# Kernel optimization log

Measured on AMD Instinct MI355X. Metric: run time of the kernel, lower is better.

## Reference

```python
import jax, jax.numpy as jnp
import numpy as np

B, S, D, H, F, E = 2, 1024, 1024, 16, 2048, 8
HD = D // H


def _ln(x, g, b, eps=1e-5):
    m = x.mean(-1, keepdims=True)
    v = ((x - m) ** 2).mean(-1, keepdims=True)
    return (x - m) / jnp.sqrt(v + eps) * g + b


def setup_inputs() -> dict:
    key = jax.random.key(0)
    ks = jax.random.split(key, 12)
    rn = lambda k, shp, s=0.02: jax.random.normal(k, shp, jnp.float32) * s
    return {
        'src': jax.random.normal(ks[0], (B, S, D), jnp.float32),
        'q_w': rn(ks[1], (D, D)),
        'k_w': rn(ks[2], (D, D)),
        'v_w': rn(ks[3], (D, D)),
        'out_w': rn(ks[4], (D, D)),
        'gate_w': rn(ks[5], (D, D)),
        'gate_b': rn(ks[6], (D,)),
        'scale_w': rn(ks[7], (H, HD)),
        'n1_g': jnp.ones((D,), jnp.float32),
        'n1_b': jnp.zeros((D,), jnp.float32),
        'n2_g': jnp.ones((D,), jnp.float32),
        'n2_b': jnp.zeros((D,), jnp.float32),
        'moe_gate_w': rn(ks[8], (D, E)),
        'moe_gate_b': jnp.zeros((E,), jnp.float32),
        'w1': rn(ks[9], (E, D, F)),
        'b1': jnp.zeros((E, F), jnp.float32),
        'ln_g': jnp.ones((E, F), jnp.float32),
        'ln_b': jnp.zeros((E, F), jnp.float32),
        'w2': rn(ks[10], (E, F, D)),
        'b2': jnp.zeros((E, D), jnp.float32),
        'res_scale': jnp.ones((E,), jnp.float32),
    }


def reference(src, q_w, k_w, v_w, out_w, gate_w, gate_b, scale_w,
              n1_g, n1_b, n2_g, n2_b, moe_gate_w, moe_gate_b,
              w1, b1, ln_g, ln_b, w2, b2, res_scale):
    b, s, d = src.shape
    h = scale_w.shape[0]
    hd = d // h
    # --- MemoAttention (gated, dynamically scaled), eval mode ---
    q = (src @ q_w).reshape(b, s, h, hd).transpose(0, 2, 1, 3)  # [b,h,s,hd]
    k = (src @ k_w).reshape(b, s, h, hd).transpose(0, 2, 1, 3)
    v = (src @ v_w).reshape(b, s, h, hd).transpose(0, 2, 1, 3)
    scores = jnp.einsum('bhqd,bhkd->bhqk', q, k) / np.float32(np.sqrt(hd))
    scale = jax.nn.sigmoid(jnp.einsum('bhsd,hd->bhs', q, scale_w)) * 2.0
    scores = scores * scale[..., None]
    aw = jax.nn.softmax(scores, axis=-1)
    out = jnp.einsum('bhqk,bhkd->bhqd', aw, v).transpose(0, 2, 1, 3).reshape(b, s, d)
    gate = jax.nn.sigmoid(out @ gate_w + gate_b)
    attn = (out * gate) @ out_w
    # --- residual + norm1 ---
    x = _ln(src + attn, n1_g, n1_b)
    # --- MoE FFN (top-2 routing; torch loop overwrites -> last (max-index) expert
    xr = x.reshape(-1, d)                      # [N, d]
    n = xr.shape[0]
    logits = xr @ moe_gate_w + moe_gate_b       # [N, E]
    top_v, top_i = jax.lax.top_k(logits, 2)
    wts = jax.nn.softmax(top_v, axis=-1)        # [N, 2]
    chosen = jnp.max(top_i, axis=-1)            # last-written expert per token

    def expert(W1, B1, G, Bt, W2, B2, rsc):
        hh = xr @ W1 + B1                       # [N, F]
        hh = jax.nn.gelu(_ln(hh, G, Bt), approximate=False)
        return (hh @ W2 + B2) * rsc + xr        # [N, d]

    outs = jax.vmap(expert)(w1, b1, ln_g, ln_b, w2, b2, res_scale)  # [E,N,d]
    sel = jnp.take_along_axis(outs.transpose(1, 0, 2), chosen[:, None, None], axis=1)[:, 0]
    moe = sel * jnp.sum(wts, axis=-1, keepdims=True)
    # --- residual + norm2 ---
    return _ln(x + moe.reshape(b, s, d), n2_g, n2_b)
```

## Files before the change

kernel.cpp:

```cpp
#include <hip/hip_runtime.h>


typedef _Float16 f16;
typedef _Float16 f16x8 __attribute__((ext_vector_type(8)));
typedef _Float16 f16x4 __attribute__((ext_vector_type(4)));
typedef float f32x4 __attribute__((ext_vector_type(4)));

constexpr int CS  = 1024;
constexpr int CD  = 1024;
constexpr int CH  = 16;
constexpr int CHD = 64;
constexpr int CF  = 2048;
constexpr int CE  = 8;
constexpr int CN  = 2048;
constexpr int CBH = 32;
constexpr int KS  = 512;
constexpr int MAXT = 48;

constexpr float LO_SCALE = 2048.f;
constexpr float LO_INV   = 1.f / 2048.f;

#define MFMA16(a, b, c) __builtin_amdgcn_mfma_f32_16x16x32_f16((a), (b), (c), 0, 0, 0)

#define TO_GBL(p) ((const __attribute__((address_space(1))) void*)(p))
#define TO_LDS(p) ((__attribute__((address_space(3))) void*)(p))
#define GLD16(g, l) __builtin_amdgcn_global_load_lds(TO_GBL(g), TO_LDS(l), 16, 0, 0)

__device__ __forceinline__ void fsplit(float v, f16 &hi, f16 &lo) {
  hi = (f16)v;
  lo = (f16)((v - (float)hi) * LO_SCALE);
}


__global__ void k_split_cvt(const float* __restrict__ in, f16* __restrict__ oh,
                            f16* __restrict__ ol, int n) {
  int i = (blockIdx.x * blockDim.x + threadIdx.x) * 4;
  if (i >= n) return;
  float4 v = *(const float4*)(in + i);
  float a[4] = {v.x, v.y, v.z, v.w};
#pragma unroll
  for (int j = 0; j < 4; ++j) {
    f16 hi = (f16)a[j];
    oh[i + j] = hi;
    ol[i + j] = (f16)((a[j] - (float)hi) * LO_SCALE);
  }
}

__global__ void k_transpose_split(const float* __restrict__ in, f16* __restrict__ oh,
                                  f16* __restrict__ ol, int R, int C) {
  __shared__ float t[32][33];
  const int z = blockIdx.z;
  const float* src = in + (size_t)z * R * C;
  f16* dh = oh + (size_t)z * R * C;
  f16* dl = ol ? ol + (size_t)z * R * C : nullptr;
  const int c0 = blockIdx.x * 32, r0 = blockIdx.y * 32;
  const int tx = threadIdx.x, ty = threadIdx.y;
#pragma unroll
  for (int i = 0; i < 32; i += 8)
    t[ty + i][tx] = src[(size_t)(r0 + ty + i) * C + c0 + tx];
  __syncthreads();
#pragma unroll
  for (int i = 0; i < 32; i += 8) {
    float v = t[tx][ty + i];
    f16 hi = (f16)v;
    size_t idx = (size_t)(c0 + ty + i) * R + r0 + tx;
    dh[idx] = hi;
    if (dl) dl[idx] = (f16)((v - (float)hi) * LO_SCALE);
  }
}


template <bool SPLIT>
__device__ __forceinline__ void gemm_tile_db(
    const f16* aH, const f16* aL, const f16* bH, const f16* bL,
    size_t bRowStride , int K, f16* lds,
    f32x4 (&accm)[2][4], f32x4 (&accc)[2][4]) {
  constexpr int BUF = SPLIT ? 12288 : 6144;
  constexpr int BOFF = SPLIT ? 4096 : 2048;
  const int t = threadIdx.x;
  const int lane = t & 63, wave = t >> 6;
  const int wm = wave >> 1, wn = wave & 1;
  const int m16 = lane & 15, quad = lane >> 4;
  int aoff[2], boff[4];
#pragma unroll
  for (int sm = 0; sm < 2; ++sm) {
    const int r = wm * 32 + sm * 16 + m16;
    aoff[sm] = r * 32 + ((quad ^ ((r >> 1) & 3)) * 8);
  }
#pragma unroll
  for (int sn = 0; sn < 4; ++sn) {
    const int r = wn * 64 + sn * 16 + m16;
    boff[sn] = BOFF + r * 32 + ((quad ^ ((r >> 1) & 3)) * 8);
  }
  auto stage = [&](f16* buf) {
    GLD16(aH, buf + t * 8);
    GLD16(bH, buf + BOFF + t * 8);
    GLD16(bH + bRowStride, buf + BOFF + 2048 + t * 8);
    if constexpr (SPLIT) {
      GLD16(aL, buf + 2048 + t * 8);
      GLD16(bL, buf + 8192 + t * 8);
      GLD16(bL + bRowStride, buf + 10240 + t * 8);
      aL += 32; bL += 32;
    }
    aH += 32; bH += 32;
  };
  stage(lds);
  int cur = 0;
  for (int k = 0; k < K; k += 32) {
    __syncthreads();
    f16* buf = lds + cur * BUF;
    if (k + 32 < K) stage(lds + (cur ^ 1) * BUF);
    f16x8 af[2], alf[2], bf[4], blf[4];
#pragma unroll
    for (int sm = 0; sm < 2; ++sm) {
      af[sm] = *(const f16x8*)(buf + aoff[sm]);
      if constexpr (SPLIT) alf[sm] = *(const f16x8*)(buf + 2048 + aoff[sm]);
    }
#pragma unroll
    for (int sn = 0; sn < 4; ++sn) {
      bf[sn] = *(const f16x8*)(buf + boff[sn]);
      if constexpr (SPLIT) blf[sn] = *(const f16x8*)(buf + 4096 + boff[sn]);
    }
#pragma unroll
    for (int sm = 0; sm < 2; ++sm)
#pragma unroll
      for (int sn = 0; sn < 4; ++sn) {
        accm[sm][sn] = MFMA16(af[sm], bf[sn], accm[sm][sn]);
        if constexpr (SPLIT) {
          accc[sm][sn] = MFMA16(af[sm], blf[sn], accc[sm][sn]);
          accc[sm][sn] = MFMA16(alf[sm], bf[sn], accc[sm][sn]);
        }
      }
    cur ^= 1;
  }
}


__global__ __launch_bounds__(256) void g_qkv(
    const f16* __restrict__ srcH, const f16* __restrict__ srcL,
    const f16* __restrict__ qwH, const f16* __restrict__ qwL,
    const f16* __restrict__ kwH, const f16* __restrict__ kwL,
    const f16* __restrict__ vwH, const f16* __restrict__ vwL,
    f16* __restrict__ qHo, f16* __restrict__ qLo,
    f16* __restrict__ kHo, f16* __restrict__ kLo,
    f16* __restrict__ vTH, f16* __restrict__ vTL) {
  __shared__ f16 lds[24576];
  const int z = blockIdx.z;
  const int m0 = blockIdx.x * 64, n0 = blockIdx.y * 128;
  const int t = threadIdx.x;
  const int rowS = t >> 2;
  const int ksw = ((t & 3) ^ ((rowS >> 1) & 3)) * 8;
  const f16* BH = (z == 0) ? qwH : (z == 1) ? kwH : vwH;
  const f16* BL = (z == 0) ? qwL : (z == 1) ? kwL : vwL;
  const f32x4 VZ = {0.f, 0.f, 0.f, 0.f};
  f32x4 accm[2][4], accc[2][4];
#pragma unroll
  for (int i = 0; i < 2; ++i)
#pragma unroll
    for (int j = 0; j < 4; ++j) { accm[i][j] = VZ; accc[i][j] = VZ; }
  gemm_tile_db<true>(srcH + (size_t)(m0 + rowS) * CD + ksw,
                     srcL + (size_t)(m0 + rowS) * CD + ksw,
                     BH + (size_t)(n0 + rowS) * CD + ksw,
                     BL + (size_t)(n0 + rowS) * CD + ksw,
                     (size_t)64 * CD, CD, lds, accm, accc);
  const int lane = t & 63, wave = t >> 6;
  const int wm = wave >> 1, wn = wave & 1;
  const int m16 = lane & 15, quad = lane >> 4;
#pragma unroll
  for (int sm = 0; sm < 2; ++sm)
#pragma unroll
    for (int sn = 0; sn < 4; ++sn)
#pragma unroll
      for (int r = 0; r < 4; ++r) {
        const int row = m0 + wm * 32 + sm * 16 + quad * 4 + r;
        const int col = n0 + wn * 64 + sn * 16 + m16;
        const float v = accm[sm][sn][r] + accc[sm][sn][r] * LO_INV;
        f16 hi, lo; fsplit(v, hi, lo);
        const int bb = row >> 10, ss = row & 1023;
        const int hh = col >> 6, hd = col & 63;
        if (z == 2) {
          const size_t idx = ((size_t)((bb * CH + hh) * CHD + hd)) * CS + ss;
          vTH[idx] = hi; vTL[idx] = lo;
        } else {
          const size_t idx = ((size_t)((bb * CH + hh) * CS + ss)) * CHD + hd;
          if (z == 0) { qHo[idx] = hi; qLo[idx] = lo; }
          else        { kHo[idx] = hi; kLo[idx] = lo; }
        }
      }
}


__device__ __forceinline__ int pswz(int q, int k) {
  return q * 64 + ((((k >> 2) ^ q) & 15) << 2) + (k & 3);
}

__global__ __launch_bounds__(256) void k_fattn(
    const f16* __restrict__ qH_, const f16* __restrict__ qL_,
    const f16* __restrict__ kH_, const f16* __restrict__ kL_,
    const f16* __restrict__ vTH_, const f16* __restrict__ vTL_,
    const float* __restrict__ scale_w,
    f16* __restrict__ aoH, f16* __restrict__ aoL) {
  __shared__ f16 kvb[32768];
  __shared__ float psc[4 * 1024];
  const int bh = blockIdx.y;
  const int b = bh >> 4, h = bh & 15;
  const int t = threadIdx.x;
  const int lane = t & 63, wave = t >> 6;
  const int m16 = lane & 15, quad = lane >> 4;
  const int q0 = blockIdx.x * 64 + wave * 16;
  float* P = psc + wave * 1024;
  const f32x4 VZ = {0.f, 0.f, 0.f, 0.f};
  const size_t kb = (size_t)bh * CS * CHD;

  const int rowS = t >> 3, chS = t & 7;
  auto stage = [&](f16* dst, int kc) {
#pragma unroll
    for (int i = 0; i < 2; ++i) {
      const int row = rowS + 32 * i;
      const int sc = (chS ^ (row & 7)) * 8;
      GLD16(kH_ + kb + (size_t)(kc + row) * CHD + sc, dst + i * 2048 + t * 8);
      GLD16(kL_ + kb + (size_t)(kc + row) * CHD + sc, dst + 4096 + i * 2048 + t * 8);
      GLD16(vTH_ + kb + (size_t)row * CS + kc + sc, dst + 8192 + i * 2048 + t * 8);
      GLD16(vTL_ + kb + (size_t)row * CS + kc + sc, dst + 12288 + i * 2048 + t * 8);
    }
  };
  auto ldf = [&](const f16* piece, int r, int q) -> f16x8 {
    return *(const f16x8*)(piece + r * 64 + ((q ^ (r & 7)) * 8));
  };

  const f16* qrh = qH_ + ((size_t)bh * CS + q0 + m16) * CHD + quad * 8;
  const f16* qrl = qL_ + ((size_t)bh * CS + q0 + m16) * CHD + quad * 8;
  f16x8 a0h = *(const f16x8*)(qrh);
  f16x8 a1h = *(const f16x8*)(qrh + 32);
  f16x8 a0l = *(const f16x8*)(qrl);
  f16x8 a1l = *(const f16x8*)(qrl + 32);

  stage(kvb, 0);

  float dot = 0.f;
  {
    const float* sw = scale_w + h * CHD + quad * 8;
    float4 s0 = *(const float4*)(sw);
    float4 s1 = *(const float4*)(sw + 4);
    float4 s2 = *(const float4*)(sw + 32);
    float4 s3 = *(const float4*)(sw + 36);
    float sv[16] = {s0.x, s0.y, s0.z, s0.w, s1.x, s1.y, s1.z, s1.w,
                    s2.x, s2.y, s2.z, s2.w, s3.x, s3.y, s3.z, s3.w};
#pragma unroll
    for (int j = 0; j < 8; ++j) {
      dot += ((float)a0h[j] + (float)a0l[j] * LO_INV) * sv[j];
      dot += ((float)a1h[j] + (float)a1l[j] * LO_INV) * sv[8 + j];
    }
    dot += __shfl_xor(dot, 16);
    dot += __shfl_xor(dot, 32);
  }
  const float qsv = 2.f / (1.f + __expf(-dot));
  float qsr[4];
#pragma unroll
  for (int r = 0; r < 4; ++r) qsr[r] = __shfl(qsv, quad * 4 + r) * 0.125f;

  f32x4 accm[4], accc[4];
#pragma unroll
  for (int tt = 0; tt < 4; ++tt) { accm[tt] = VZ; accc[tt] = VZ; }
  float mrun[4], lrun[4];
#pragma unroll
  for (int r = 0; r < 4; ++r) { mrun[r] = -1e30f; lrun[r] = 0.f; }

  int cur = 0;
  for (int kc = 0; kc < CS; kc += 64) {
    __syncthreads();
    const f16* kv = kvb + cur * 16384;
    if (kc + 64 < CS) stage(kvb + (cur ^ 1) * 16384, kc + 64);

    f32x4 st[4];
#pragma unroll
    for (int tt = 0; tt < 4; ++tt) {
      const int r = tt * 16 + m16;
      f16x8 b0h = ldf(kv,        r, quad);
      f16x8 b1h = ldf(kv,        r, quad + 4);
      f16x8 b0l = ldf(kv + 4096, r, quad);
      f16x8 b1l = ldf(kv + 4096, r, quad + 4);
      f32x4 am = VZ, ac = VZ;
      am = MFMA16(a0h, b0h, am); am = MFMA16(a1h, b1h, am);
      ac = MFMA16(a0h, b0l, ac); ac = MFMA16(a0l, b0h, ac);
      ac = MFMA16(a1h, b1l, ac); ac = MFMA16(a1l, b1h, ac);
#pragma unroll
      for (int r4 = 0; r4 < 4; ++r4)
        st[tt][r4] = (am[r4] + ac[r4] * LO_INV) * qsr[r4];
    }
    float alpha[4];
#pragma unroll
    for (int r = 0; r < 4; ++r) {
      float mx = fmaxf(fmaxf(st[0][r], st[1][r]), fmaxf(st[2][r], st[3][r]));
#pragma unroll
      for (int msk = 8; msk >= 1; msk >>= 1) mx = fmaxf(mx, __shfl_xor(mx, msk));
      const float mnew = fmaxf(mrun[r], mx);
      alpha[r] = __expf(mrun[r] - mnew);
      mrun[r] = mnew;
    }
    float rs[4] = {0.f, 0.f, 0.f, 0.f};
#pragma unroll
    for (int tt = 0; tt < 4; ++tt)
#pragma unroll
      for (int r = 0; r < 4; ++r) {
        const float e = __expf(st[tt][r] - mrun[r]);
        rs[r] += e;
        P[pswz(quad * 4 + r, tt * 16 + m16)] = e;
      }
#pragma unroll
    for (int r = 0; r < 4; ++r) {
#pragma unroll
      for (int msk = 8; msk >= 1; msk >>= 1) rs[r] += __shfl_xor(rs[r], msk);
      lrun[r] = lrun[r] * alpha[r] + rs[r];
#pragma unroll
      for (int tt = 0; tt < 4; ++tt) { accm[tt][r] *= alpha[r]; accc[tt][r] *= alpha[r]; }
    }
    f16x8 pah[2], pal[2];
#pragma unroll
    for (int c = 0; c < 2; ++c) {
      const int k0 = c * 32 + quad * 8;
      float4 p0 = *(const float4*)(P + pswz(m16, k0));
      float4 p1 = *(const float4*)(P + pswz(m16, k0 + 4));
      float pv[8] = {p0.x, p0.y, p0.z, p0.w, p1.x, p1.y, p1.z, p1.w};
#pragma unroll
      for (int j = 0; j < 8; ++j) {
        f16 hi = (f16)pv[j];
        pah[c][j] = hi;
        pal[c][j] = (f16)((pv[j] - (float)hi) * LO_SCALE);
      }
    }
#pragma unroll
    for (int tt = 0; tt < 4; ++tt) {
      const int r = tt * 16 + m16;
#pragma unroll
      for (int c = 0; c < 2; ++c) {
        f16x8 vbh = ldf(kv + 8192,  r, quad + 4 * c);
        f16x8 vbl = ldf(kv + 12288, r, quad + 4 * c);
        accm[tt] = MFMA16(pah[c], vbh, accm[tt]);
        accc[tt] = MFMA16(pah[c], vbl, accc[tt]);
        accc[tt] = MFMA16(pal[c], vbh, accc[tt]);
      }
    }
    cur ^= 1;
  }
#pragma unroll
  for (int tt = 0; tt < 4; ++tt)
#pragma unroll
    for (int r = 0; r < 4; ++r) {
      const int row = q0 + quad * 4 + r;
      const float v = (accm[tt][r] + accc[tt][r] * LO_INV) / lrun[r];
      f16 hi, lo; fsplit(v, hi, lo);
      const size_t idx = ((size_t)(b * CS + row)) * CD + h * CHD + tt * 16 + m16;
      aoH[idx] = hi; aoL[idx] = lo;
    }
}


__global__ __launch_bounds__(256) void g_gate(
    const f16* __restrict__ aoH, const f16* __restrict__ aoL,
    const f16* __restrict__ gwH, const f16* __restrict__ gwL,
    float* __restrict__ gpre ) {
  __shared__ f16 lds[24576];
  const int m0 = blockIdx.x * 64, n0 = blockIdx.y * 128, s = blockIdx.z;
  const int t = threadIdx.x;
  const int rowS = t >> 2;
  const int ksw = ((t & 3) ^ ((rowS >> 1) & 3)) * 8;
  const int k0 = s * KS;
  const f32x4 VZ = {0.f, 0.f, 0.f, 0.f};
  f32x4 accm[2][4], accc[2][4];
#pragma unroll
  for (int i = 0; i < 2; ++i)
#pragma unroll
    for (int j = 0; j < 4; ++j) { accm[i][j] = VZ; accc[i][j] = VZ; }
  gemm_tile_db<true>(aoH + (size_t)(m0 + rowS) * CD + k0 + ksw,
                     aoL + (size_t)(m0 + rowS) * CD + k0 + ksw,
                     gwH + (size_t)(n0 + rowS) * CD + k0 + ksw,
                     gwL + (size_t)(n0 + rowS) * CD + k0 + ksw,
                     (size_t)64 * CD, KS, lds, accm, accc);
  float* gp = gpre + (size_t)s * CN * CD;
  const int lane = t & 63, wave = t >> 6;
  const int wm = wave >> 1, wn = wave & 1;
  const int m16 = lane & 15, quad = lane >> 4;
#pragma unroll
  for (int sm = 0; sm < 2; ++sm)
#pragma unroll
    for (int sn = 0; sn < 4; ++sn)
#pragma unroll
      for (int r = 0; r < 4; ++r) {
        const int row = m0 + wm * 32 + sm * 16 + quad * 4 + r;
        const int col = n0 + wn * 64 + sn * 16 + m16;
        gp[(size_t)row * CD + col] = accm[sm][sn][r] + accc[sm][sn][r] * LO_INV;
      }
}

__global__ __launch_bounds__(256) void k_gatemul(
    const float* __restrict__ gpre, const f16* __restrict__ aoH,
    const f16* __restrict__ aoL, const float* __restrict__ gate_b,
    f16* __restrict__ gdH, f16* __restrict__ gdL) {
  const int i = (blockIdx.x * 256 + threadIdx.x) * 4;
  float4 p0 = *(const float4*)(gpre + i);
  float4 p1 = *(const float4*)(gpre + (size_t)CN * CD + i);
  float4 gb = *(const float4*)(gate_b + (i & (CD - 1)));
  f16x4 ah = *(const f16x4*)(aoH + i);
  f16x4 al = *(const f16x4*)(aoL + i);
  float pre[4] = {p0.x + p1.x + gb.x, p0.y + p1.y + gb.y,
                  p0.z + p1.z + gb.z, p0.w + p1.w + gb.w};
  f16x4 oh, ol;
#pragma unroll
  for (int j = 0; j < 4; ++j) {
    const float g = 1.f / (1.f + __expf(-pre[j]));
    const float ov = ((float)ah[j] + (float)al[j] * LO_INV) * g;
    f16 hi, lo; fsplit(ov, hi, lo);
    oh[j] = hi; ol[j] = lo;
  }
  *(f16x4*)(gdH + i) = oh;
  *(f16x4*)(gdL + i) = ol;
}

__global__ __launch_bounds__(256) void g_outp(
    const f16* __restrict__ gdH, const f16* __restrict__ gdL,
    const f16* __restrict__ owH, const f16* __restrict__ owL,
    float* __restrict__ y1p ) {
  __shared__ f16 lds[24576];
  const int m0 = blockIdx.x * 64, n0 = blockIdx.y * 128, s = blockIdx.z;
  const int t = threadIdx.x;
  const int rowS = t >> 2;
  const int ksw = ((t & 3) ^ ((rowS >> 1) & 3)) * 8;
  const int k0 = s * KS;
  const f32x4 VZ = {0.f, 0.f, 0.f, 0.f};
  f32x4 accm[2][4], accc[2][4];
#pragma unroll
  for (int i = 0; i < 2; ++i)
#pragma unroll
    for (int j = 0; j < 4; ++j) { accm[i][j] = VZ; accc[i][j] = VZ; }
  gemm_tile_db<true>(gdH + (size_t)(m0 + rowS) * CD + k0 + ksw,
                     gdL + (size_t)(m0 + rowS) * CD + k0 + ksw,
                     owH + (size_t)(n0 + rowS) * CD + k0 + ksw,
                     owL + (size_t)(n0 + rowS) * CD + k0 + ksw,
                     (size_t)64 * CD, KS, lds, accm, accc);
  float* yp = y1p + (size_t)s * CN * CD;
  const int lane = t & 63, wave = t >> 6;
  const int wm = wave >> 1, wn = wave & 1;
  const int m16 = lane & 15, quad = lane >> 4;
#pragma unroll
  for (int sm = 0; sm < 2; ++sm)
#pragma unroll
    for (int sn = 0; sn < 4; ++sn)
#pragma unroll
      for (int r = 0; r < 4; ++r) {
        const int row = m0 + wm * 32 + sm * 16 + quad * 4 + r;
        const int col = n0 + wn * 64 + sn * 16 + m16;
        yp[(size_t)row * CD + col] = accm[sm][sn][r] + accc[sm][sn][r] * LO_INV;
      }
}


__device__ __forceinline__ void block_reduce2(float &s, float &ss, float* red) {
#pragma unroll
  for (int msk = 32; msk >= 1; msk >>= 1) {
    s += __shfl_xor(s, msk);
    ss += __shfl_xor(ss, msk);
  }
  const int wave = threadIdx.x >> 6, lane = threadIdx.x & 63;
  if (lane == 0) { red[wave] = s; red[4 + wave] = ss; }
  __syncthreads();
  s = red[0] + red[1] + red[2] + red[3];
  ss = red[4] + red[5] + red[6] + red[7];
}

__global__ __launch_bounds__(256) void k_ln1(
    const float* __restrict__ y1p, const float* __restrict__ srcp,
    const float* __restrict__ g, const float* __restrict__ bb,
    float* __restrict__ x, f16* __restrict__ xH) {
  __shared__ float red[8];
  const int n = blockIdx.x;
  const int t = threadIdx.x;
  const size_t off = (size_t)n * CD + t * 4;
  float4 v0 = *(const float4*)(y1p + off);
  float4 v1 = *(const float4*)(y1p + (size_t)CN * CD + off);
  float4 v2 = *(const float4*)(srcp + off);
  float a[4] = {v0.x + v1.x + v2.x, v0.y + v1.y + v2.y,
                v0.z + v1.z + v2.z, v0.w + v1.w + v2.w};
  float s = a[0] + a[1] + a[2] + a[3];
  float ss = a[0]*a[0] + a[1]*a[1] + a[2]*a[2] + a[3]*a[3];
  block_reduce2(s, ss, red);
  const float mean = s * (1.f / CD);
  const float var = ss * (1.f / CD) - mean * mean;
  const float rstd = rsqrtf(var + 1e-5f);
#pragma unroll
  for (int j = 0; j < 4; ++j) {
    const int d = t * 4 + j;
    const float val = (a[j] - mean) * rstd * g[d] + bb[d];
    x[(size_t)n * CD + d] = val;
    xH[(size_t)n * CD + d] = (f16)val;
  }
}

__global__ __launch_bounds__(256) void k_ln2(
    const float* __restrict__ zbp, const float* __restrict__ x,
    const float* __restrict__ b2, const float* __restrict__ rsc,
    const int* __restrict__ chosen,
    const float* __restrict__ g, const float* __restrict__ bb,
    float* __restrict__ outp) {
  __shared__ float red[8];
  const int n = blockIdx.x;
  const int e = chosen[n];
  const float rs = rsc[e];
  const int t = threadIdx.x;
  const size_t off = (size_t)n * CD + t * 4;
  float4 p0 = *(const float4*)(zbp + off);
  float4 p1 = *(const float4*)(zbp + (size_t)CN * CD + off);
  float4 p2 = *(const float4*)(zbp + (size_t)2 * CN * CD + off);
  float4 p3 = *(const float4*)(zbp + (size_t)3 * CN * CD + off);
  float4 xv = *(const float4*)(x + off);
  float4 bv = *(const float4*)(b2 + (size_t)e * CD + t * 4);
  float a[4] = {2.f * xv.x + (p0.x + p1.x + p2.x + p3.x + bv.x) * rs,
                2.f * xv.y + (p0.y + p1.y + p2.y + p3.y + bv.y) * rs,
                2.f * xv.z + (p0.z + p1.z + p2.z + p3.z + bv.z) * rs,
                2.f * xv.w + (p0.w + p1.w + p2.w + p3.w + bv.w) * rs};
  float s = a[0] + a[1] + a[2] + a[3];
  float ss = a[0]*a[0] + a[1]*a[1] + a[2]*a[2] + a[3]*a[3];
  block_reduce2(s, ss, red);
  const float mean = s * (1.f / CD);
  const float var = ss * (1.f / CD) - mean * mean;
  const float rstd = rsqrtf(var + 1e-5f);
#pragma unroll
  for (int j = 0; j < 4; ++j) {
    const int d = t * 4 + j;
    outp[(size_t)n * CD + d] = (a[j] - mean) * rstd * g[d] + bb[d];
  }
}


__global__ void k_zero_counts(int* counts) {
  if (threadIdx.x < CE) counts[threadIdx.x] = 0;
}

__global__ __launch_bounds__(256) void k_route(
    const float* __restrict__ x, const float* __restrict__ gw, const float* __restrict__ gb,
    int* __restrict__ chosen, int* __restrict__ counts, int* __restrict__ bucket) {
  const int wave = threadIdx.x >> 6, lane = threadIdx.x & 63;
  const int n = blockIdx.x * 4 + wave;
  const float* xr = x + (size_t)n * CD;
  float acc[CE];
#pragma unroll
  for (int e = 0; e < CE; ++e) acc[e] = 0.f;
  for (int j = 0; j < 16; ++j) {
    const int d = lane * 16 + j;
    const float xv = xr[d];
    const float* wr = gw + (size_t)d * CE;
#pragma unroll
    for (int e = 0; e < CE; ++e) acc[e] += xv * wr[e];
  }
#pragma unroll
  for (int msk = 32; msk >= 1; msk >>= 1) {
#pragma unroll
    for (int e = 0; e < CE; ++e) acc[e] += __shfl_xor(acc[e], msk);
  }
  if (lane == 0) {
    float best = -1e30f, second = -1e30f;
    int bi = 0, si = 0;
#pragma unroll
    for (int e = 0; e < CE; ++e) {
      const float L = acc[e] + gb[e];
      if (L > best) { second = best; si = bi; best = L; bi = e; }
      else if (L > second) { second = L; si = e; }
    }
    const int ch = bi > si ? bi : si;
    chosen[n] = ch;
    const int pos = atomicAdd(&counts[ch], 1);
    bucket[ch * CN + pos] = n;
  }
}

__global__ void k_plan(const int* __restrict__ counts, int* __restrict__ tiles) {
  if (threadIdx.x == 0) {
    int n = 0;
    for (int e = 0; e < CE; ++e) {
      const int c = counts[e];
      for (int m0 = 0; m0 < c; m0 += 64) { tiles[2 * n] = e; tiles[2 * n + 1] = m0; ++n; }
    }
    for (; n < MAXT; ++n) { tiles[2 * n] = -1; tiles[2 * n + 1] = 0; }
  }
}


__global__ __launch_bounds__(256) void g_moe1(
    const f16* __restrict__ xH, const f16* __restrict__ w1t,
    const int* __restrict__ counts, const int* __restrict__ bucket,
    const int* __restrict__ tiles, float* __restrict__ hbp ) {
  const int e = tiles[2 * blockIdx.x];
  if (e < 0) return;
  const int m0 = tiles[2 * blockIdx.x + 1];
  const int cnt = counts[e];
  const int s = blockIdx.z;
  __shared__ f16 lds[12288];
  const int t = threadIdx.x;
  const int rowS = t >> 2;
  const int ksw = ((t & 3) ^ ((rowS >> 1) & 3)) * 8;
  const int k0 = s * KS;
  int ra = m0 + rowS; if (ra > cnt - 1) ra = cnt - 1;
  const int tokA = bucket[e * CN + ra];
  const int n0 = blockIdx.y * 128;
  const f32x4 VZ = {0.f, 0.f, 0.f, 0.f};
  f32x4 accm[2][4], accd[2][4];
#pragma unroll
  for (int i = 0; i < 2; ++i)
#pragma unroll
    for (int j = 0; j < 4; ++j) { accm[i][j] = VZ; accd[i][j] = VZ; }
  gemm_tile_db<false>(xH + (size_t)tokA * CD + k0 + ksw, nullptr,
                      w1t + ((size_t)e * CF + n0 + rowS) * CD + k0 + ksw, nullptr,
                      (size_t)64 * CD, KS, lds, accm, accd);
  float* hp = hbp + (size_t)s * CN * CF;
  const int lane = t & 63, wave = t >> 6;
  const int wm = wave >> 1, wn = wave & 1;
  const int m16 = lane & 15, quad = lane >> 4;
#pragma unroll
  for (int sm = 0; sm < 2; ++sm)
#pragma unroll
    for (int sn = 0; sn < 4; ++sn)
#pragma unroll
      for (int r = 0; r < 4; ++r) {
        const int rr = m0 + wm * 32 + sm * 16 + quad * 4 + r;
        if (rr >= cnt) continue;
        const int tok = bucket[e * CN + rr];
        const int col = n0 + wn * 64 + sn * 16 + m16;
        hp[(size_t)tok * CF + col] = accm[sm][sn][r];
      }
}

__global__ __launch_bounds__(256) void k_lngelu(
    const float* __restrict__ hbp, const int* __restrict__ chosen,
    const float* __restrict__ b1,
    const float* __restrict__ ln_g, const float* __restrict__ ln_b,
    f16* __restrict__ h2) {
  __shared__ float red[8];
  const int n = blockIdx.x;
  const int e = chosen[n];
  const int t = threadIdx.x;
  const size_t off = (size_t)n * CF + t * 8;
  float4 v0 = *(const float4*)(hbp + off);
  float4 v1 = *(const float4*)(hbp + off + 4);
  float4 u0 = *(const float4*)(hbp + (size_t)CN * CF + off);
  float4 u1 = *(const float4*)(hbp + (size_t)CN * CF + off + 4);
  float4 b0 = *(const float4*)(b1 + (size_t)e * CF + t * 8);
  float4 b1v = *(const float4*)(b1 + (size_t)e * CF + t * 8 + 4);
  float a[8] = {v0.x + u0.x + b0.x, v0.y + u0.y + b0.y,
                v0.z + u0.z + b0.z, v0.w + u0.w + b0.w,
                v1.x + u1.x + b1v.x, v1.y + u1.y + b1v.y,
                v1.z + u1.z + b1v.z, v1.w + u1.w + b1v.w};
  float s = 0.f, ss = 0.f;
#pragma unroll
  for (int j = 0; j < 8; ++j) { s += a[j]; ss += a[j] * a[j]; }
  block_reduce2(s, ss, red);
  const float mean = s * (1.f / CF);
  const float var = ss * (1.f / CF) - mean * mean;
  const float rstd = rsqrtf(var + 1e-5f);
  const float* g = ln_g + (size_t)e * CF;
  const float* bb = ln_b + (size_t)e * CF;
#pragma unroll
  for (int j = 0; j < 8; ++j) {
    const int d = t * 8 + j;
    const float val = (a[j] - mean) * rstd * g[d] + bb[d];
    const float gl = 0.5f * val * (1.f + erff(val * 0.70710678118654752f));
    h2[(size_t)n * CF + d] = (f16)gl;
  }
}

__global__ __launch_bounds__(256) void g_moe2(
    const f16* __restrict__ h2, const f16* __restrict__ w2t,
    const int* __restrict__ counts, const int* __restrict__ bucket,
    const int* __restrict__ tiles, float* __restrict__ zbp ) {
  const int e = tiles[2 * blockIdx.x];
  if (e < 0) return;
  const int m0 = tiles[2 * blockIdx.x + 1];
  const int cnt = counts[e];
  const int s = blockIdx.z;
  __shared__ f16 lds[12288];
  const int t = threadIdx.x;
  const int rowS = t >> 2;
  const int ksw = ((t & 3) ^ ((rowS >> 1) & 3)) * 8;
  const int k0 = s * KS;
  int ra = m0 + rowS; if (ra > cnt - 1) ra = cnt - 1;
  const int tokA = bucket[e * CN + ra];
  const int n0 = blockIdx.y * 128;
  const f32x4 VZ = {0.f, 0.f, 0.f, 0.f};
  f32x4 accm[2][4], accd[2][4];
#pragma unroll
  for (int i = 0; i < 2; ++i)
#pragma unroll
    for (int j = 0; j < 4; ++j) { accm[i][j] = VZ; accd[i][j] = VZ; }
  gemm_tile_db<false>(h2 + (size_t)tokA * CF + k0 + ksw, nullptr,
                      w2t + ((size_t)e * CD + n0 + rowS) * CF + k0 + ksw, nullptr,
                      (size_t)64 * CF, KS, lds, accm, accd);
  float* zp = zbp + (size_t)s * CN * CD;
  const int lane = t & 63, wave = t >> 6;
  const int wm = wave >> 1, wn = wave & 1;
  const int m16 = lane & 15, quad = lane >> 4;
#pragma unroll
  for (int sm = 0; sm < 2; ++sm)
#pragma unroll
    for (int sn = 0; sn < 4; ++sn)
#pragma unroll
      for (int r = 0; r < 4; ++r) {
        const int rr = m0 + wm * 32 + sm * 16 + quad * 4 + r;
        if (rr >= cnt) continue;
        const int tok = bucket[e * CN + rr];
        const int col = n0 + wn * 64 + sn * 16 + m16;
        zp[(size_t)tok * CD + col] = accm[sm][sn][r];
      }
}


extern "C" void kernel_launch(void* const* d_in, const int* in_sizes, int n_in,
                              void* d_out, int out_size, void* d_ws, size_t ws_size,
                              hipStream_t stream) {
  (void)in_sizes; (void)n_in; (void)out_size; (void)ws_size;
  const float* src        = (const float*)d_in[0];
  const float* q_w        = (const float*)d_in[1];
  const float* k_w        = (const float*)d_in[2];
  const float* v_w        = (const float*)d_in[3];
  const float* out_w      = (const float*)d_in[4];
  const float* gate_w     = (const float*)d_in[5];
  const float* gate_b     = (const float*)d_in[6];
  const float* scale_w    = (const float*)d_in[7];
  const float* n1_g       = (const float*)d_in[8];
  const float* n1_b       = (const float*)d_in[9];
  const float* n2_g       = (const float*)d_in[10];
  const float* n2_b       = (const float*)d_in[11];
  const float* moe_gate_w = (const float*)d_in[12];
  const float* moe_gate_b = (const float*)d_in[13];
  const float* w1         = (const float*)d_in[14];
  const float* b1         = (const float*)d_in[15];
  const float* ln_g       = (const float*)d_in[16];
  const float* ln_b       = (const float*)d_in[17];
  const float* w2         = (const float*)d_in[18];
  const float* b2         = (const float*)d_in[19];
  const float* res_scale  = (const float*)d_in[20];
  float* outp = (float*)d_out;

  char* p = (char*)d_ws;
  auto take = [&](size_t bytes) -> char* {
    char* r = p;
    p += (bytes + 255) & ~(size_t)255;
    return r;
  };
  f16* srcH = (f16*)take((size_t)CN * CD * 2);
  f16* srcL = (f16*)take((size_t)CN * CD * 2);
  f16* qwH = (f16*)take((size_t)CD * CD * 2);
  f16* qwL = (f16*)take((size_t)CD * CD * 2);
  f16* kwH = (f16*)take((size_t)CD * CD * 2);
  f16* kwL = (f16*)take((size_t)CD * CD * 2);
  f16* vwH = (f16*)take((size_t)CD * CD * 2);
  f16* vwL = (f16*)take((size_t)CD * CD * 2);
  f16* gwH = (f16*)take((size_t)CD * CD * 2);
  f16* gwL = (f16*)take((size_t)CD * CD * 2);
  f16* owH = (f16*)take((size_t)CD * CD * 2);
  f16* owL = (f16*)take((size_t)CD * CD * 2);
  f16* qH = (f16*)take((size_t)CBH * CS * CHD * 2);
  f16* qL = (f16*)take((size_t)CBH * CS * CHD * 2);
  f16* kH = (f16*)take((size_t)CBH * CS * CHD * 2);
  f16* kL = (f16*)take((size_t)CBH * CS * CHD * 2);
  f16* vTH = (f16*)take((size_t)CBH * CS * CHD * 2);
  f16* vTL = (f16*)take((size_t)CBH * CS * CHD * 2);
  f16* aoH = (f16*)take((size_t)CN * CD * 2);
  f16* aoL = (f16*)take((size_t)CN * CD * 2);
  f16* gdH = (f16*)take((size_t)CN * CD * 2);
  f16* gdL = (f16*)take((size_t)CN * CD * 2);
  float* x  = (float*)take((size_t)CN * CD * 4);
  f16* xH = (f16*)take((size_t)CN * CD * 2);
  int* counts = (int*)take(64);
  int* bucket = (int*)take((size_t)CE * CN * 4);
  int* chosen = (int*)take((size_t)CN * 4);
  int* tiles = (int*)take((size_t)MAXT * 2 * 4);
  f16* h2 = (f16*)take((size_t)CN * CF * 2);
  f16* w1t = (f16*)take((size_t)CE * CF * CD * 2);
  f16* w2t = (f16*)take((size_t)CE * CD * CF * 2);
  float* pbuf = (float*)take((size_t)4 * CN * CD * 4);

  k_split_cvt<<<dim3(CN * CD / 4 / 256), 256, 0, stream>>>(src, srcH, srcL, CN * CD);
  dim3 tb(32, 8);
  k_transpose_split<<<dim3(CD / 32, CD / 32, 1), tb, 0, stream>>>(q_w, qwH, qwL, CD, CD);
  k_transpose_split<<<dim3(CD / 32, CD / 32, 1), tb, 0, stream>>>(k_w, kwH, kwL, CD, CD);
  k_transpose_split<<<dim3(CD / 32, CD / 32, 1), tb, 0, stream>>>(v_w, vwH, vwL, CD, CD);
  k_transpose_split<<<dim3(CD / 32, CD / 32, 1), tb, 0, stream>>>(gate_w, gwH, gwL, CD, CD);
  k_transpose_split<<<dim3(CD / 32, CD / 32, 1), tb, 0, stream>>>(out_w, owH, owL, CD, CD);
  k_transpose_split<<<dim3(CF / 32, CD / 32, CE), tb, 0, stream>>>(w1, w1t, nullptr, CD, CF);
  k_transpose_split<<<dim3(CD / 32, CF / 32, CE), tb, 0, stream>>>(w2, w2t, nullptr, CF, CD);

  g_qkv<<<dim3(CN / 64, CD / 128, 3), 256, 0, stream>>>(
      srcH, srcL, qwH, qwL, kwH, kwL, vwH, vwL, qH, qL, kH, kL, vTH, vTL);
  k_fattn<<<dim3(CS / 64, CBH), 256, 0, stream>>>(
      qH, qL, kH, kL, vTH, vTL, scale_w, aoH, aoL);
  g_gate<<<dim3(CN / 64, CD / 128, 2), 256, 0, stream>>>(aoH, aoL, gwH, gwL, pbuf);
  k_gatemul<<<dim3(CN * CD / 4 / 256), 256, 0, stream>>>(pbuf, aoH, aoL, gate_b, gdH, gdL);
  g_outp<<<dim3(CN / 64, CD / 128, 2), 256, 0, stream>>>(gdH, gdL, owH, owL, pbuf);
  k_ln1<<<dim3(CN), 256, 0, stream>>>(pbuf, src, n1_g, n1_b, x, xH);

  k_zero_counts<<<dim3(1), 64, 0, stream>>>(counts);
  k_route<<<dim3(CN / 4), 256, 0, stream>>>(x, moe_gate_w, moe_gate_b, chosen, counts, bucket);
  k_plan<<<dim3(1), 64, 0, stream>>>(counts, tiles);
  g_moe1<<<dim3(40, CF / 128, 2), 256, 0, stream>>>(xH, w1t, counts, bucket, tiles, pbuf);
  k_lngelu<<<dim3(CN), 256, 0, stream>>>(pbuf, chosen, b1, ln_g, ln_b, h2);
  g_moe2<<<dim3(40, CD / 128, 4), 256, 0, stream>>>(h2, w2t, counts, bucket, tiles, pbuf);
  k_ln2<<<dim3(CN), 256, 0, stream>>>(pbuf, x, b2, res_scale, chosen, n2_g, n2_b, outp);
}
```

Before: 535.7 us.

## Triple-buffer GEMM LDS staging and vectorize split/transpose conversion kernels

The shared GEMM tile routine moves from double to triple buffering. It issues two stages ahead and uses explicit vmcnt waits plus a raw barrier instead of __syncthreads, so more global-to-LDS loads stay in flight while the MFMAs run. The LDS allocations of all GEMM kernels grow by half to hold the third buffer, which may reduce occupancy. The split-convert and transpose-split kernels now write vectorized f16x4 stores, and the transpose uses 64x64 tiles with 256 threads, which cuts store instruction count for the weight preprocessing.

```diff
diff --git a/kernel.cpp b/kernel.cpp
--- a/kernel.cpp
+++ b/kernel.cpp
@@ -38,34 +38,47 @@
   if (i >= n) return;
   float4 v = *(const float4*)(in + i);
   float a[4] = {v.x, v.y, v.z, v.w};
+  f16x4 vh, vl;
 #pragma unroll
   for (int j = 0; j < 4; ++j) {
     f16 hi = (f16)a[j];
-    oh[i + j] = hi;
-    ol[i + j] = (f16)((a[j] - (float)hi) * LO_SCALE);
-  }
-}
-
-__global__ void k_transpose_split(const float* __restrict__ in, f16* __restrict__ oh,
-                                  f16* __restrict__ ol, int R, int C) {
-  __shared__ float t[32][33];
+    vh[j] = hi;
+    vl[j] = (f16)((a[j] - (float)hi) * LO_SCALE);
+  }
+  *(f16x4*)(oh + i) = vh;
+  *(f16x4*)(ol + i) = vl;
+}
+
+__global__ __launch_bounds__(256) void k_transpose_split(
+    const float* __restrict__ in, f16* __restrict__ oh,
+    f16* __restrict__ ol, int R, int C) {
+  __shared__ float t[64][65];
   const int z = blockIdx.z;
   const float* src = in + (size_t)z * R * C;
   f16* dh = oh + (size_t)z * R * C;
   f16* dl = ol ? ol + (size_t)z * R * C : nullptr;
-  const int c0 = blockIdx.x * 32, r0 = blockIdx.y * 32;
-  const int tx = threadIdx.x, ty = threadIdx.y;
-#pragma unroll
-  for (int i = 0; i < 32; i += 8)
-    t[ty + i][tx] = src[(size_t)(r0 + ty + i) * C + c0 + tx];
+  const int c0 = blockIdx.x * 64, r0 = blockIdx.y * 64;
+  const int tt = threadIdx.x;
+  const int lane = tt & 63, wv = tt >> 6;
+#pragma unroll
+  for (int i = 0; i < 16; ++i)
+    t[wv + i * 4][lane] = src[(size_t)(r0 + wv + i * 4) * C + c0 + lane];
   __syncthreads();
-#pragma unroll
-  for (int i = 0; i < 32; i += 8) {
-    float v = t[tx][ty + i];
-    f16 hi = (f16)v;
-    size_t idx = (size_t)(c0 + ty + i) * R + r0 + tx;
-    dh[idx] = hi;
-    if (dl) dl[idx] = (f16)((v - (float)hi) * LO_SCALE);
+  const int oc = tt >> 4;
+  const int og = tt & 15;
+#pragma unroll
+  for (int cc = 0; cc < 64; cc += 16) {
+    f16x4 vh, vl;
+#pragma unroll
+    for (int j = 0; j < 4; ++j) {
+      const float v = t[og * 4 + j][cc + oc];
+      f16 hi = (f16)v;
+      vh[j] = hi;
+      vl[j] = (f16)((v - (float)hi) * LO_SCALE);
+    }
+    const size_t idx = (size_t)(c0 + cc + oc) * R + r0 + og * 4;
+    *(f16x4*)(dh + idx) = vh;
+    if (dl) *(f16x4*)(dl + idx) = vl;
   }
 }
 
@@ -105,11 +118,22 @@
     aH += 32; bH += 32;
   };
   stage(lds);
+  stage(lds + BUF);
   int cur = 0;
   for (int k = 0; k < K; k += 32) {
-    __syncthreads();
+    if (k + 32 < K) {
+      if constexpr (SPLIT) asm volatile("s_waitcnt vmcnt(6)" ::: "memory");
+      else                 asm volatile("s_waitcnt vmcnt(3)" ::: "memory");
+    } else {
+      asm volatile("s_waitcnt vmcnt(0)" ::: "memory");
+    }
+    __builtin_amdgcn_s_barrier();
+    asm volatile("" ::: "memory");
     f16* buf = lds + cur * BUF;
-    if (k + 32 < K) stage(lds + (cur ^ 1) * BUF);
+    if (k + 64 < K) {
+      int pf = cur + 2; if (pf >= 3) pf -= 3;
+      stage(lds + pf * BUF);
+    }
     f16x8 af[2], alf[2], bf[4], blf[4];
 #pragma unroll
     for (int sm = 0; sm < 2; ++sm) {
@@ -131,7 +155,7 @@
           accc[sm][sn] = MFMA16(alf[sm], bf[sn], accc[sm][sn]);
         }
       }
-    cur ^= 1;
+    if (++cur == 3) cur = 0;
   }
 }
 
@@ -144,7 +168,7 @@
     f16* __restrict__ qHo, f16* __restrict__ qLo,
     f16* __restrict__ kHo, f16* __restrict__ kLo,
     f16* __restrict__ vTH, f16* __restrict__ vTL) {
-  __shared__ f16 lds[24576];
+  __shared__ f16 lds[36864];
   const int z = blockIdx.z;
   const int m0 = blockIdx.x * 64, n0 = blockIdx.y * 128;
   const int t = threadIdx.x;
@@ -360,7 +384,7 @@
     const f16* __restrict__ aoH, const f16* __restrict__ aoL,
     const f16* __restrict__ gwH, const f16* __restrict__ gwL,
     float* __restrict__ gpre ) {
-  __shared__ f16 lds[24576];
+  __shared__ f16 lds[36864];
   const int m0 = blockIdx.x * 64, n0 = blockIdx.y * 128, s = blockIdx.z;
   const int t = threadIdx.x;
   const int rowS = t >> 2;
@@ -421,7 +445,7 @@
     const f16* __restrict__ gdH, const f16* __restrict__ gdL,
     const f16* __restrict__ owH, const f16* __restrict__ owL,
     float* __restrict__ y1p ) {
-  __shared__ f16 lds[24576];
+  __shared__ f16 lds[36864];
   const int m0 = blockIdx.x * 64, n0 = blockIdx.y * 128, s = blockIdx.z;
   const int t = threadIdx.x;
   const int rowS = t >> 2;
@@ -594,7 +618,7 @@
   const int m0 = tiles[2 * blockIdx.x + 1];
   const int cnt = counts[e];
   const int s = blockIdx.z;
-  __shared__ f16 lds[12288];
+  __shared__ f16 lds[18432];
   const int t = threadIdx.x;
   const int rowS = t >> 2;
   const int ksw = ((t & 3) ^ ((rowS >> 1) & 3)) * 8;
@@ -676,7 +700,7 @@
   const int m0 = tiles[2 * blockIdx.x + 1];
   const int cnt = counts[e];
   const int s = blockIdx.z;
-  __shared__ f16 lds[12288];
+  __shared__ f16 lds[18432];
   const int t = threadIdx.x;
   const int rowS = t >> 2;
   const int ksw = ((t & 3) ^ ((rowS >> 1) & 3)) * 8;
@@ -779,14 +803,13 @@
   float* pbuf = (float*)take((size_t)4 * CN * CD * 4);
 
   k_split_cvt<<<dim3(CN * CD / 4 / 256), 256, 0, stream>>>(src, srcH, srcL, CN * CD);
-  dim3 tb(32, 8);
-  k_transpose_split<<<dim3(CD / 32, CD / 32, 1), tb, 0, stream>>>(q_w, qwH, qwL, CD, CD);
-  k_transpose_split<<<dim3(CD / 32, CD / 32, 1), tb, 0, stream>>>(k_w, kwH, kwL, CD, CD);
-  k_transpose_split<<<dim3(CD / 32, CD / 32, 1), tb, 0, stream>>>(v_w, vwH, vwL, CD, CD);
-  k_transpose_split<<<dim3(CD / 32, CD / 32, 1), tb, 0, stream>>>(gate_w, gwH, gwL, CD, CD);
-  k_transpose_split<<<dim3(CD / 32, CD / 32, 1), tb, 0, stream>>>(out_w, owH, owL, CD, CD);
-  k_transpose_split<<<dim3(CF / 32, CD / 32, CE), tb, 0, stream>>>(w1, w1t, nullptr, CD, CF);
-  k_transpose_split<<<dim3(CD / 32, CF / 32, CE), tb, 0, stream>>>(w2, w2t, nullptr, CF, CD);
+  k_transpose_split<<<dim3(CD / 64, CD / 64, 1), 256, 0, stream>>>(q_w, qwH, qwL, CD, CD);
+  k_transpose_split<<<dim3(CD / 64, CD / 64, 1), 256, 0, stream>>>(k_w, kwH, kwL, CD, CD);
+  k_transpose_split<<<dim3(CD / 64, CD / 64, 1), 256, 0, stream>>>(v_w, vwH, vwL, CD, CD);
+  k_transpose_split<<<dim3(CD / 64, CD / 64, 1), 256, 0, stream>>>(gate_w, gwH, gwL, CD, CD);
+  k_transpose_split<<<dim3(CD / 64, CD / 64, 1), 256, 0, stream>>>(out_w, owH, owL, CD, CD);
+  k_transpose_split<<<dim3(CF / 64, CD / 64, CE), 256, 0, stream>>>(w1, w1t, nullptr, CD, CF);
+  k_transpose_split<<<dim3(CD / 64, CF / 64, CE), 256, 0, stream>>>(w2, w2t, nullptr, CF, CD);
 
   g_qkv<<<dim3(CN / 64, CD / 128, 3), 256, 0, stream>>>(
       srcH, srcL, qwH, qwL, kwH, kwL, vwH, vwL, qH, qL, kH, kL, vTH, vTL);
```

New measurement: 533.7 us. About the same (-0.4%).
